# Optimization experiments

Measured on AMD Instinct MI355X. Metric: run time of the kernel, lower is better.

The kernel has to match this reference:

```python
import jax, jax.numpy as jnp
import numpy as np
from jax import lax

NK, NV, DK, DV, K, C = 16, 32, 128, 128, 4, 2048
KEY_DIM = NK * DK
VAL_DIM = NV * DV
CONV_DIM = 2 * KEY_DIM + VAL_DIM
EPS = 1e-6


def setup_inputs() -> dict:
    key = jax.random.key(0)
    ks = jax.random.split(key, 10)
    B, T = 2, 2048
    s = 0.02
    return {
        "x": jax.random.normal(ks[0], (B, T, C), jnp.float32),
        "input_pos": jnp.arange(T, dtype=jnp.int32),
        "W_qkv": jax.random.normal(ks[1], (CONV_DIM, C), jnp.float32) * s,
        "W_z": jax.random.normal(ks[2], (VAL_DIM, C), jnp.float32) * s,
        "W_b": jax.random.normal(ks[3], (NV, C), jnp.float32) * s,
        "W_a": jax.random.normal(ks[4], (NV, C), jnp.float32) * s,
        "conv_w": jax.random.normal(ks[5], (CONV_DIM, 1, K), jnp.float32) * 0.1,
        "dt_bias": jnp.ones((NV,), jnp.float32),
        "A_log": jnp.log(jax.random.uniform(ks[6], (NV,), jnp.float32, 1e-3, 16.0)),
        "norm_w": jnp.ones((DV,), jnp.float32),
        "W_out": jax.random.normal(ks[7], (C, VAL_DIM), jnp.float32) * s,
        "conv_state": jnp.zeros((B, CONV_DIM, K), jnp.float32),
        "recurrent_state": jnp.zeros((B, NV, DK, DV), jnp.float32),
    }


def reference(x, input_pos, W_qkv, W_z, W_b, W_a, conv_w, dt_bias, A_log,
              norm_w, W_out, conv_state, recurrent_state):
    B, T, _ = x.shape
    # reset cached state when starting a new sequence (input_pos[0] == 0)
    keep = 1.0 - (input_pos[0] == 0).astype(x.dtype)
    conv_state = conv_state * keep
    state0 = recurrent_state * keep

    qkv = jnp.einsum('btc,dc->btd', x, W_qkv)                      # [B,T,CONV_DIM]
    z = jnp.einsum('btc,dc->btd', x, W_z).reshape(B, T, NV, DV)
    beta = jax.nn.sigmoid(jnp.einsum('btc,hc->bth', x, W_b))       # [B,T,NV]
    a = jnp.einsum('btc,hc->bth', x, W_a)
    g = -jnp.exp(A_log) * jax.nn.softplus(a + dt_bias)             # [B,T,NV]

    # causal depthwise conv using cached conv_state as left context
    conv_in = jnp.concatenate([conv_state, qkv.transpose(0, 2, 1)], axis=-1)  # [B,D,K+T]
    conv_out = lax.conv_general_dilated(
        conv_in, conv_w, (1,), 'VALID',
        dimension_numbers=('NCH', 'OIH', 'NCH'),
        feature_group_count=CONV_DIM)
    qkv_c = jax.nn.silu(conv_out[:, :, -T:]).transpose(0, 2, 1)    # [B,T,CONV_DIM]

    q = qkv_c[..., :KEY_DIM].reshape(B, T, NK, DK)
    k = qkv_c[..., KEY_DIM:2 * KEY_DIM].reshape(B, T, NK, DK)
    v = qkv_c[..., 2 * KEY_DIM:].reshape(B, T, NV, DV)
    q = q / jnp.maximum(jnp.linalg.norm(q, axis=-1, keepdims=True), 1e-12)
    k = k / jnp.maximum(jnp.linalg.norm(k, axis=-1, keepdims=True), 1e-12)
    rep = NV // NK
    if rep > 1:
        q = jnp.repeat(q, rep, axis=2)
        k = jnp.repeat(k, rep, axis=2)

    # gated delta-rule recurrence over time
    def step(carry, xs):
        q_i, k_i, v_i, g_i, b_i = xs                               # [B,H,*]
        new = (jnp.exp(g_i)[..., None, None] * carry
               + b_i[..., None, None] * (k_i[..., :, None] * v_i[..., None, :]))
        out = jnp.einsum('bhk,bhkv->bhv', q_i, new)
        return new, out

    xs = (q.transpose(1, 0, 2, 3), k.transpose(1, 0, 2, 3),
          v.transpose(1, 0, 2, 3), g.transpose(1, 0, 2), beta.transpose(1, 0, 2))
    state, outs = lax.scan(step, state0, xs)
    o = outs.transpose(1, 0, 2, 3)                                 # [B,T,NV,DV]

    # gated RMSNorm (Mamba2-style): gate with silu(z), then RMS-normalize
    o = o * jax.nn.silu(z)
    var = jnp.mean(o * o, axis=-1, keepdims=True)
    o = o * lax.rsqrt(var + EPS) * norm_w
    return jnp.einsum('btd,cd->btc', o.reshape(B, T, VAL_DIM), W_out)
```

## Files before the change

### kernel.cpp

```cpp
#include <hip/hip_runtime.h>
#include <hip/hip_bf16.h>
#include <math.h>

#define NKH 16
#define NVH 32
#define DKD 128
#define DVD 128
#define CDIM 2048
#define KEY_DIM 2048
#define VAL_DIM 4096
#define CONV_DIM 8192
#define BB 2
#define TT 2048
#define MROWS 4096
#define CH 64
#define NCHUNK 32

typedef unsigned short u16;
typedef __bf16 bf16x8 __attribute__((ext_vector_type(8)));
typedef float f32x4 __attribute__((ext_vector_type(4)));

__device__ __forceinline__ u16 f2bf(float f) {
    union { float f; unsigned u; } a; a.f = f;
    unsigned u = a.u;
    u += 0x7fffu + ((u >> 16) & 1u);
    return (u16)(u >> 16);
}
__device__ __forceinline__ float bf2f(u16 h) {
    union { unsigned u; float f; } a; a.u = ((unsigned)h) << 16;
    return a.f;
}
union BF8 { bf16x8 v; uint2 u2[2]; uint4 u4; u16 s[8]; };
__device__ __forceinline__ bf16x8 lds_ld8(const u16* p) {
    BF8 t; t.u2[0] = *(const uint2*)p; t.u2[1] = *(const uint2*)(p + 4); return t.v;
}
__device__ __forceinline__ bf16x8 lds_ld16(const u16* p) {
    BF8 t; t.u4 = *(const uint4*)p; return t.v;
}
__device__ __forceinline__ void lds_st8(u16* p, uint4 v) {
    *(uint2*)p = make_uint2(v.x, v.y); *(uint2*)(p + 4) = make_uint2(v.z, v.w);
}

__device__ __forceinline__ void xcd_swizzle(int& tx, int& ty) {
    const int nx = gridDim.x, ny = gridDim.y;
    const int b  = blockIdx.x + nx * blockIdx.y;
    const int nb = nx * ny;
    if (nx >= 8 && (nx & 7) == 0 && (nb & 255) == 0) {
        const int rnd  = b >> 8;
        const int idx  = b & 255;
        const int xcd  = idx & 7;
        const int slot = idx >> 3;
        const int RX   = nx >> 3;
        const int rx   = xcd & (RX - 1);
        const int ry   = xcd >> __popc(RX - 1);
        tx = rx * 8 + (slot & 7);
        ty = rnd * (256 / nx) + ry * 4 + (slot >> 3);
    } else {
        tx = blockIdx.x; ty = blockIdx.y;
    }
}

__global__ __launch_bounds__(256) void fill_kernel(float* __restrict__ p, float v, int n) {
    int i = blockIdx.x * 256 + threadIdx.x;
    if (i < n) p[i] = v;
}

__global__ __launch_bounds__(256) void cast_kernel(const float* __restrict__ src,
                                                   u16* __restrict__ dst, int n4) {
    int i = blockIdx.x * 256 + threadIdx.x;
    if (i >= n4) return;
    float4 v = ((const float4*)src)[i];
    ushort4 r;
    r.x = f2bf(v.x); r.y = f2bf(v.y); r.z = f2bf(v.z); r.w = f2bf(v.w);
    ((ushort4*)dst)[i] = r;
}

template<int OUT_BF16>
__global__ __launch_bounds__(256) void gemm_nt(const u16* __restrict__ A,
                                               const u16* __restrict__ Bm,
                                               void* __restrict__ Cv,
                                               int M, int N, int K) {
    __shared__ __align__(16) u16 As[128 * 64];
    __shared__ __align__(16) u16 Bs[128 * 64];
    const int tid  = threadIdx.x;
    const int lane = tid & 63;
    const int wave = tid >> 6;
    int tx, ty;
    xcd_swizzle(tx, ty);
    const int m0 = ty * 128;
    const int n0 = tx * 128;
    const int wm = (wave & 1) * 64;
    const int wn = (wave >> 1) * 64;
    const int l15  = lane & 15;
    const int quad = lane >> 4;

    f32x4 acc[4][4];
#pragma unroll
    for (int i = 0; i < 4; ++i)
#pragma unroll
        for (int j = 0; j < 4; ++j) acc[i][j] = (f32x4)0.0f;

    const int crow = tid >> 3;
    const int ccol = (tid & 7) * 8;

    for (int k0 = 0; k0 < K; k0 += 64) {
#pragma unroll
        for (int p = 0; p < 4; ++p) {
            int row = p * 32 + crow;
            const u16* ga = A + (size_t)(m0 + row) * K + k0 + ccol;
            char* la = (char*)As + (size_t)(p * 256 + (wave << 6)) * 16;
            __builtin_amdgcn_global_load_lds((const __attribute__((address_space(1))) void*)ga,
                                             (__attribute__((address_space(3))) void*)la, 16, 0, 0);
            const u16* gb = Bm + (size_t)(n0 + row) * K + k0 + ccol;
            char* lb = (char*)Bs + (size_t)(p * 256 + (wave << 6)) * 16;
            __builtin_amdgcn_global_load_lds((const __attribute__((address_space(1))) void*)gb,
                                             (__attribute__((address_space(3))) void*)lb, 16, 0, 0);
        }
        __syncthreads();
#pragma unroll
        for (int kk = 0; kk < 64; kk += 32) {
            bf16x8 af[4], bfr[4];
#pragma unroll
            for (int i = 0; i < 4; ++i) {
                af[i]  = *(const bf16x8*)&As[(wm + i * 16 + l15) * 64 + kk + quad * 8];
                bfr[i] = *(const bf16x8*)&Bs[(wn + i * 16 + l15) * 64 + kk + quad * 8];
            }
#pragma unroll
            for (int i = 0; i < 4; ++i)
#pragma unroll
                for (int j = 0; j < 4; ++j)
                    acc[i][j] = __builtin_amdgcn_mfma_f32_16x16x32_bf16(af[i], bfr[j], acc[i][j], 0, 0, 0);
        }
        __syncthreads();
    }
#pragma unroll
    for (int i = 0; i < 4; ++i) {
#pragma unroll
        for (int j = 0; j < 4; ++j) {
#pragma unroll
            for (int r = 0; r < 4; ++r) {
                int grow = m0 + wm + i * 16 + quad * 4 + r;
                int gcol = n0 + wn + j * 16 + l15;
                if (OUT_BF16) {
                    ((u16*)Cv)[(size_t)grow * N + gcol] = f2bf(acc[i][j][r]);
                } else {
                    ((float*)Cv)[(size_t)grow * N + gcol] = acc[i][j][r];
                }
            }
        }
    }
}

template<int OUT_BF16>
__global__ __launch_bounds__(512, 2) void gemm_nt_256(const u16* __restrict__ A,
                                                      const u16* __restrict__ Bm,
                                                      void* __restrict__ Cv,
                                                      int M, int N, int K) {
    __shared__ __align__(16) u16 sA[2][256 * 64];
    __shared__ __align__(16) u16 sB[2][256 * 64];
    const int tid  = threadIdx.x;
    const int lane = tid & 63;
    const int wave = tid >> 6;
    const int wr   = wave >> 2;
    const int wc   = wave & 3;
    const int l15  = lane & 15;
    const int quad = lane >> 4;
    int tx, ty;
    xcd_swizzle(tx, ty);
    const int m0 = ty * 256;
    const int n0 = tx * 256;

    f32x4 acc[8][4];
#pragma unroll
    for (int i = 0; i < 8; ++i)
#pragma unroll
        for (int j = 0; j < 4; ++j) acc[i][j] = (f32x4)0.0f;

    auto stage = [&](int buf, int kk0) {
#pragma unroll
        for (int p = 0; p < 4; ++p) {
            const int gbase = p * 512 + wave * 64;
            const int g   = gbase + lane;
            const int row = g >> 3;
            const int sc  = (g & 7) ^ (row & 7);
            const u16* ga = A + (size_t)(m0 + row) * K + kk0 + sc * 8;
            __builtin_amdgcn_global_load_lds(
                (const __attribute__((address_space(1))) void*)ga,
                (__attribute__((address_space(3))) void*)((char*)&sA[buf][0] + (size_t)gbase * 16),
                16, 0, 0);
            const u16* gb = Bm + (size_t)(n0 + row) * K + kk0 + sc * 8;
            __builtin_amdgcn_global_load_lds(
                (const __attribute__((address_space(1))) void*)gb,
                (__attribute__((address_space(3))) void*)((char*)&sB[buf][0] + (size_t)gbase * 16),
                16, 0, 0);
        }
    };

    const int NT = K >> 6;
    stage(0, 0);

    for (int T = 0; T < NT; ++T) {
        const int P = T & 1;
        __builtin_amdgcn_sched_barrier(0);
        asm volatile("s_waitcnt vmcnt(0)" ::: "memory");
        __builtin_amdgcn_s_barrier();
        __builtin_amdgcn_sched_barrier(0);
        if (T + 1 < NT) stage(P ^ 1, (T + 1) << 6);

        bf16x8 bB[4][2];
#pragma unroll
        for (int j = 0; j < 4; ++j)
#pragma unroll
            for (int kk = 0; kk < 2; ++kk) {
                int row  = wc * 64 + j * 16 + l15;
                int slot = ((kk * 4 + quad) ^ (l15 & 7)) * 8;
                bB[j][kk] = lds_ld16(&sB[P][row * 64 + slot]);
            }
        bf16x8 aC[2][2], aN[2][2];
#pragma unroll
        for (int i = 0; i < 2; ++i)
#pragma unroll
            for (int kk = 0; kk < 2; ++kk) {
                int row  = wr * 128 + i * 16 + l15;
                int slot = ((kk * 4 + quad) ^ (l15 & 7)) * 8;
                aC[i][kk] = lds_ld16(&sA[P][row * 64 + slot]);
            }

#pragma unroll
        for (int q = 0; q < 4; ++q) {
            if (q < 3) {
#pragma unroll
                for (int i = 0; i < 2; ++i)
#pragma unroll
                    for (int kk = 0; kk < 2; ++kk) {
                        int row  = wr * 128 + ((q + 1) * 2 + i) * 16 + l15;
                        int slot = ((kk * 4 + quad) ^ (l15 & 7)) * 8;
                        aN[i][kk] = lds_ld16(&sA[P][row * 64 + slot]);
                    }
            }
            __builtin_amdgcn_s_setprio(1);
#pragma unroll
            for (int i = 0; i < 2; ++i)
#pragma unroll
                for (int j = 0; j < 4; ++j)
#pragma unroll
                    for (int kk = 0; kk < 2; ++kk)
                        acc[q * 2 + i][j] = __builtin_amdgcn_mfma_f32_16x16x32_bf16(
                            aC[i][kk], bB[j][kk], acc[q * 2 + i][j], 0, 0, 0);
            __builtin_amdgcn_s_setprio(0);
            __builtin_amdgcn_sched_barrier(0);
            if (q < 3) {
                __builtin_amdgcn_s_barrier();
#pragma unroll
                for (int i = 0; i < 2; ++i)
#pragma unroll
                    for (int kk = 0; kk < 2; ++kk) aC[i][kk] = aN[i][kk];
            }
        }
    }

#pragma unroll
    for (int i = 0; i < 8; ++i) {
#pragma unroll
        for (int j = 0; j < 4; ++j) {
#pragma unroll
            for (int r = 0; r < 4; ++r) {
                int grow = m0 + wr * 128 + i * 16 + quad * 4 + r;
                int gcol = n0 + wc * 64 + j * 16 + l15;
                if (OUT_BF16) {
                    ((u16*)Cv)[(size_t)grow * N + gcol] = f2bf(acc[i][j][r]);
                } else {
                    ((float*)Cv)[(size_t)grow * N + gcol] = acc[i][j][r];
                }
            }
        }
    }
}

__global__ __launch_bounds__(256) void bg_epilogue(const float* __restrict__ scores,
                                                   const float* __restrict__ dt_bias,
                                                   const float* __restrict__ A_log,
                                                   float* __restrict__ beta,
                                                   float* __restrict__ g) {
    int i = blockIdx.x * 256 + threadIdx.x;
    int row = i >> 6, col = i & 63;
    float s = scores[(size_t)row * 128 + col];
    if (col < 32) {
        beta[(size_t)row * 32 + col] = 1.f / (1.f + __expf(-s));
    } else {
        int h = col - 32;
        float aa = s + dt_bias[h];
        float sp = (aa > 20.f) ? aa : log1pf(__expf(aa));
        g[(size_t)row * 32 + h] = -__expf(A_log[h]) * sp;
    }
}

__global__ __launch_bounds__(256) void conv_silu_kernel(const u16* __restrict__ qkv,
                                                        const float* __restrict__ conv_w,
                                                        const float* __restrict__ conv_state,
                                                        const int* __restrict__ input_pos,
                                                        u16* __restrict__ qkvc) {
    const int d   = blockIdx.x * 256 + threadIdx.x;
    const int row = blockIdx.y;
    const int t   = row & (TT - 1);
    const int b   = row >> 11;
    const float keep = (input_pos[0] == 0) ? 0.f : 1.f;
    float4 w = *(const float4*)&conv_w[(size_t)d * 4];
    float acc = 0.f;
#pragma unroll
    for (int j = 0; j < 4; ++j) {
        int u = t + j - 3;
        float v;
        if (u >= 0) v = bf2f(qkv[(size_t)(b * TT + u) * CONV_DIM + d]);
        else        v = keep * conv_state[((size_t)b * CONV_DIM + d) * 4 + (u + 4)];
        acc += (&w.x)[j] * v;
    }
    float s = acc / (1.f + __expf(-acc));
    qkvc[(size_t)row * CONV_DIM + d] = f2bf(s);
}

__global__ __launch_bounds__(256) void qknorm_kernel(u16* __restrict__ qkvc) {
    const int gid  = blockIdx.x * 4 + (threadIdx.x >> 6);
    const int lane = threadIdx.x & 63;
    const int row  = gid >> 5;
    const int h    = gid & 31;
    u16* p = qkvc + (size_t)row * CONV_DIM + h * 128;
    ushort2 vb = *(ushort2*)&p[lane * 2];
    float v0 = bf2f(vb.x), v1 = bf2f(vb.y);
    float ss = v0 * v0 + v1 * v1;
#pragma unroll
    for (int off = 32; off; off >>= 1) ss += __shfl_xor(ss, off);
    float scale = 1.f / fmaxf(sqrtf(ss), 1e-12f);
    ushort2 r;
    r.x = f2bf(v0 * scale);
    r.y = f2bf(v1 * scale);
    *(ushort2*)&p[lane * 2] = r;
}

__global__ __launch_bounds__(64) void gates_kernel(const float* __restrict__ g,
                                                   const float* __restrict__ beta_,
                                                   float* __restrict__ gcum,
                                                   float* __restrict__ qsb,
                                                   float* __restrict__ wkb,
                                                   float* __restrict__ dLb) {
    const int bh = blockIdx.x, c = blockIdx.y;
    const int b = bh >> 5, h = bh & 31;
    const int t = threadIdx.x;
    const int row = b * TT + c * CH + t;
    float G = g[(size_t)row * 32 + h];
#pragma unroll
    for (int off = 1; off < 64; off <<= 1) {
        float x = __shfl_up(G, off);
        if (t >= off) G += x;
    }
    float GL = __shfl(G, 63);
    int oidx = bh * TT + c * CH + t;
    gcum[oidx] = G;
    qsb[oidx] = __expf(G);
    wkb[oidx] = __expf(GL - G) * beta_[(size_t)row * 32 + h];
    if (t == 0) dLb[bh * NCHUNK + c] = __expf(GL);
}

__global__ __launch_bounds__(256) void ktrans_kernel(const u16* __restrict__ qkvc,
                                                     u16* __restrict__ kT) {
    const int id = blockIdx.x;
    const int tt = id & 31, dkh = (id >> 5) & 1, hk = (id >> 6) & 15, b = id >> 10;
    const int t0 = tt * 64, dk0 = dkh * 64;
    __shared__ __align__(16) u16 tile[64 * 68];
#pragma unroll
    for (int it = 0; it < 2; ++it) {
        int idx = it * 256 + threadIdx.x;
        int tl = idx >> 3, c8 = (idx & 7) * 8;
        uint4 v = *(const uint4*)&qkvc[(size_t)(b * TT + t0 + tl) * CONV_DIM + KEY_DIM + hk * 128 + dk0 + c8];
        lds_st8(&tile[tl * 68 + c8], v);
    }
    __syncthreads();
#pragma unroll
    for (int it = 0; it < 2; ++it) {
        int idx = it * 256 + threadIdx.x;
        int dkl = idx >> 3, t8 = (idx & 7) * 8;
        unsigned w[4];
#pragma unroll
        for (int p = 0; p < 4; ++p) {
            unsigned lo = tile[(t8 + 2 * p) * 68 + dkl];
            unsigned hi = tile[(t8 + 2 * p + 1) * 68 + dkl];
            w[p] = lo | (hi << 16);
        }
        *(uint4*)&kT[((size_t)((b * 16 + hk) * 128 + dk0 + dkl)) * TT + t0 + t8] =
            make_uint4(w[0], w[1], w[2], w[3]);
    }
}

__global__ __launch_bounds__(256) void chunk_state_kernel(const u16* __restrict__ qkvc,
                                                          const u16* __restrict__ kT,
                                                          const float* __restrict__ qsb,
                                                          const float* __restrict__ wkb,
                                                          const float* __restrict__ dLb,
                                                          const float* __restrict__ rec_state,
                                                          const int* __restrict__ input_pos,
                                                          u16* __restrict__ o) {
    const int b = blockIdx.x, h = blockIdx.y, dvs = blockIdx.z;
    const int tid = threadIdx.x, lane = tid & 63, wave = tid >> 6;
    const int l15 = lane & 15, quad = lane >> 4;
    const int hq = h >> 1, bh = b * 32 + h;
    const float keep = (input_pos[0] == 0) ? 0.f : 1.f;

    __shared__ __align__(16) u16 sQ[64 * 132];
    __shared__ __align__(16) u16 sKT[128 * 68];
    __shared__ __align__(16) u16 sR[32 * 132];
    __shared__ float sQS[64];

    f32x4 st[2][2];
#pragma unroll
    for (int i = 0; i < 2; ++i)
#pragma unroll
        for (int j = 0; j < 2; ++j)
#pragma unroll
            for (int r = 0; r < 4; ++r) {
                int dv = dvs * 32 + i * 16 + quad * 4 + r;
                int dk = wave * 32 + j * 16 + l15;
                st[i][j][r] = keep * rec_state[((size_t)(bh * 128 + dk)) * 128 + dv];
            }

    for (int c = 0; c < NCHUNK; ++c) {
        const int t0 = c * CH;
#pragma unroll
        for (int i = 0; i < 2; ++i)
#pragma unroll
            for (int j = 0; j < 2; ++j)
#pragma unroll
                for (int r = 0; r < 4; ++r)
                    sR[(i * 16 + quad * 4 + r) * 132 + wave * 32 + j * 16 + l15] = f2bf(st[i][j][r]);
#pragma unroll
        for (int it = 0; it < 4; ++it) {
            int idx = it * 256 + tid;
            int t = idx >> 4, c8 = (idx & 15) * 8;
            uint4 v = *(const uint4*)&qkvc[(size_t)(b * TT + t0 + t) * CONV_DIM + hq * 128 + c8];
            lds_st8(&sQ[t * 132 + c8], v);
        }
        if (tid < 64) sQS[tid] = qsb[bh * TT + t0 + tid];
        __syncthreads();
        {
            f32x4 ao[2] = {(f32x4)0.0f, (f32x4)0.0f};
#pragma unroll
            for (int kk = 0; kk < 4; ++kk) {
                bf16x8 af = lds_ld8(&sQ[(wave * 16 + l15) * 132 + kk * 32 + quad * 8]);
                bf16x8 b0 = lds_ld8(&sR[(l15) * 132 + kk * 32 + quad * 8]);
                bf16x8 b1 = lds_ld8(&sR[(16 + l15) * 132 + kk * 32 + quad * 8]);
                ao[0] = __builtin_amdgcn_mfma_f32_16x16x32_bf16(af, b0, ao[0], 0, 0, 0);
                ao[1] = __builtin_amdgcn_mfma_f32_16x16x32_bf16(af, b1, ao[1], 0, 0, 0);
            }
#pragma unroll
            for (int j = 0; j < 2; ++j)
#pragma unroll
                for (int r = 0; r < 4; ++r) {
                    int t = wave * 16 + quad * 4 + r;
                    int dv = dvs * 32 + j * 16 + l15;
                    o[((size_t)(b * TT + t0 + t) * 32 + h) * 128 + dv] = f2bf(ao[j][r] * sQS[t]);
                }
        }
        __syncthreads();
#pragma unroll
        for (int it = 0; it < 4; ++it) {
            int idx = it * 256 + tid;
            int dk = idx >> 3, t8 = (idx & 7) * 8;
            uint4 v = *(const uint4*)&kT[((size_t)((b * 16 + hq) * 128 + dk)) * TT + t0 + t8];
            lds_st8(&sKT[dk * 68 + t8], v);
        }
        {
            int t = tid >> 2, dvo = (tid & 3) * 8;
            float w = wkb[bh * TT + t0 + t];
            BF8 v;
            v.u4 = *(const uint4*)&qkvc[(size_t)(b * TT + t0 + t) * CONV_DIM + 2 * KEY_DIM + h * 128 + dvs * 32 + dvo];
#pragma unroll
            for (int u = 0; u < 8; ++u)
                sR[(dvo + u) * 68 + t] = f2bf(bf2f(v.s[u]) * w);
        }
        __syncthreads();
        {
            float d = dLb[bh * NCHUNK + c];
#pragma unroll
            for (int i = 0; i < 2; ++i)
#pragma unroll
                for (int j = 0; j < 2; ++j)
#pragma unroll
                    for (int r = 0; r < 4; ++r) st[i][j][r] *= d;
#pragma unroll
            for (int kk = 0; kk < 2; ++kk) {
                bf16x8 af[2], bfv[2];
#pragma unroll
                for (int i = 0; i < 2; ++i)
                    af[i] = lds_ld8(&sR[(i * 16 + l15) * 68 + kk * 32 + quad * 8]);
#pragma unroll
                for (int j = 0; j < 2; ++j)
                    bfv[j] = lds_ld8(&sKT[(wave * 32 + j * 16 + l15) * 68 + kk * 32 + quad * 8]);
#pragma unroll
                for (int i = 0; i < 2; ++i)
#pragma unroll
                    for (int j = 0; j < 2; ++j)
                        st[i][j] = __builtin_amdgcn_mfma_f32_16x16x32_bf16(af[i], bfv[j], st[i][j], 0, 0, 0);
            }
        }
        __syncthreads();
    }
}

__global__ __launch_bounds__(256) void chunk_intra_kernel(const u16* __restrict__ qkvc,
                                                          const float* __restrict__ gcum,
                                                          const float* __restrict__ beta_,
                                                          u16* __restrict__ o) {
    const int b = blockIdx.x, h = blockIdx.y, c = blockIdx.z;
    const int tid = threadIdx.x, lane = tid & 63, wave = tid >> 6;
    const int l15 = lane & 15, quad = lane >> 4;
    const int hq = h >> 1, bh = b * 32 + h;
    const int t0 = c * CH;

    __shared__ __align__(16) u16 sQ[64 * 132];
    __shared__ __align__(16) u16 sK[64 * 132];
    __shared__ __align__(16) u16 sVT[128 * 68];
    __shared__ float sG[64];
    __shared__ float sB[64];

#pragma unroll
    for (int it = 0; it < 4; ++it) {
        int idx = it * 256 + tid;
        int t = idx >> 4, c8 = (idx & 15) * 8;
        size_t rbase = (size_t)(b * TT + t0 + t) * CONV_DIM;
        lds_st8(&sQ[t * 132 + c8], *(const uint4*)&qkvc[rbase + hq * 128 + c8]);
        lds_st8(&sK[t * 132 + c8], *(const uint4*)&qkvc[rbase + KEY_DIM + hq * 128 + c8]);
    }
    if (tid < 64) {
        sG[tid] = gcum[bh * TT + t0 + tid];
        sB[tid] = beta_[(size_t)(b * TT + t0 + tid) * 32 + h];
    }
    __syncthreads();
    const int wm = (wave & 1) * 32, wn = (wave >> 1) * 32;
    f32x4 acc[2][2];
#pragma unroll
    for (int i = 0; i < 2; ++i)
#pragma unroll
        for (int j = 0; j < 2; ++j) acc[i][j] = (f32x4)0.0f;
#pragma unroll
    for (int kk = 0; kk < 4; ++kk) {
        bf16x8 af[2], bfv[2];
#pragma unroll
        for (int i = 0; i < 2; ++i) {
            af[i]  = lds_ld8(&sQ[(wm + i * 16 + l15) * 132 + kk * 32 + quad * 8]);
            bfv[i] = lds_ld8(&sK[(wn + i * 16 + l15) * 132 + kk * 32 + quad * 8]);
        }
#pragma unroll
        for (int i = 0; i < 2; ++i)
#pragma unroll
            for (int j = 0; j < 2; ++j)
                acc[i][j] = __builtin_amdgcn_mfma_f32_16x16x32_bf16(af[i], bfv[j], acc[i][j], 0, 0, 0);
    }
    __syncthreads();
#pragma unroll
    for (int i = 0; i < 2; ++i)
#pragma unroll
        for (int j = 0; j < 2; ++j)
#pragma unroll
            for (int r = 0; r < 4; ++r) {
                int t = wm + i * 16 + quad * 4 + r;
                int s = wn + j * 16 + l15;
                float av = 0.f;
                if (s <= t) av = __expf(sG[t] - sG[s]) * sB[s] * acc[i][j][r];
                ((u16*)sQ)[t * 68 + s] = f2bf(av);
            }
#pragma unroll
    for (int it = 0; it < 4; ++it) {
        int idx = it * 256 + tid;
        int t = idx >> 4, c8 = (idx & 15) * 8;
        lds_st8(&sK[t * 132 + c8],
                *(const uint4*)&qkvc[(size_t)(b * TT + t0 + t) * CONV_DIM + 2 * KEY_DIM + h * 128 + c8]);
    }
    __syncthreads();
    {
        int dv = (wave & 1) * 64 + lane;
        int tb = (wave >> 1) * 32;
#pragma unroll
        for (int tc = 0; tc < 4; ++tc) {
            int t8 = tb + tc * 8;
            unsigned w[4];
#pragma unroll
            for (int p = 0; p < 4; ++p) {
                unsigned lo = sK[(t8 + 2 * p) * 132 + dv];
                unsigned hi = sK[(t8 + 2 * p + 1) * 132 + dv];
                w[p] = lo | (hi << 16);
            }
            lds_st8(&sVT[dv * 68 + t8], make_uint4(w[0], w[1], w[2], w[3]));
        }
    }
    __syncthreads();
    const int wm2 = (wave & 1) * 32, wn2 = (wave >> 1) * 64;
    f32x4 oacc[2][4];
#pragma unroll
    for (int i = 0; i < 2; ++i)
#pragma unroll
        for (int j = 0; j < 4; ++j) oacc[i][j] = (f32x4)0.0f;
#pragma unroll
    for (int kk = 0; kk < 2; ++kk) {
        bf16x8 af[2], bfv[4];
#pragma unroll
        for (int i = 0; i < 2; ++i)
            af[i] = lds_ld8(&((u16*)sQ)[(wm2 + i * 16 + l15) * 68 + kk * 32 + quad * 8]);
#pragma unroll
        for (int j = 0; j < 4; ++j)
            bfv[j] = lds_ld8(&sVT[(wn2 + j * 16 + l15) * 68 + kk * 32 + quad * 8]);
#pragma unroll
        for (int i = 0; i < 2; ++i)
#pragma unroll
            for (int j = 0; j < 4; ++j)
                oacc[i][j] = __builtin_amdgcn_mfma_f32_16x16x32_bf16(af[i], bfv[j], oacc[i][j], 0, 0, 0);
    }
#pragma unroll
    for (int i = 0; i < 2; ++i)
#pragma unroll
        for (int j = 0; j < 4; ++j)
#pragma unroll
            for (int r = 0; r < 4; ++r) {
                int t = wm2 + i * 16 + quad * 4 + r;
                int dv = wn2 + j * 16 + l15;
                size_t addr = ((size_t)(b * TT + t0 + t) * 32 + h) * 128 + dv;
                o[addr] = f2bf(oacc[i][j][r] + bf2f(o[addr]));
            }
}

__global__ __launch_bounds__(256) void gnorm_kernel(const u16* __restrict__ o,
                                                    const u16* __restrict__ zb,
                                                    const float* __restrict__ norm_w,
                                                    u16* __restrict__ ob) {
    const int gid  = blockIdx.x * 4 + (threadIdx.x >> 6);
    const int lane = threadIdx.x & 63;
    const int row  = gid >> 5;
    const int h    = gid & 31;
    const size_t base = ((size_t)row * NVH + h) * DVD;
    ushort2 oraw = *(const ushort2*)&o[base + lane * 2];
    float o0 = bf2f(oraw.x), o1 = bf2f(oraw.y);
    float z0 = bf2f(zb[base + lane * 2]);
    float z1 = bf2f(zb[base + lane * 2 + 1]);
    o0 *= z0 / (1.f + __expf(-z0));
    o1 *= z1 / (1.f + __expf(-z1));
    float ss = o0 * o0 + o1 * o1;
#pragma unroll
    for (int off = 32; off; off >>= 1) ss += __shfl_xor(ss, off);
    float scale = rsqrtf(ss * (1.f / 128.f) + 1e-6f);
    float w0 = norm_w[lane * 2], w1 = norm_w[lane * 2 + 1];
    ushort2 r;
    r.x = f2bf(o0 * scale * w0);
    r.y = f2bf(o1 * scale * w1);
    *(ushort2*)&ob[base + lane * 2] = r;
}

extern "C" void kernel_launch(void* const* d_in, const int* in_sizes, int n_in,
                              void* d_out, int out_size, void* d_ws, size_t ws_size,
                              hipStream_t stream) {
    const float* x         = (const float*)d_in[0];
    const int*   input_pos = (const int*)d_in[1];
    const float* W_qkv     = (const float*)d_in[2];
    const float* W_z       = (const float*)d_in[3];
    const float* W_b       = (const float*)d_in[4];
    const float* W_a       = (const float*)d_in[5];
    const float* conv_w    = (const float*)d_in[6];
    const float* dt_bias   = (const float*)d_in[7];
    const float* A_log     = (const float*)d_in[8];
    const float* norm_w    = (const float*)d_in[9];
    const float* W_out     = (const float*)d_in[10];
    const float* conv_state = (const float*)d_in[11];
    const float* rec_state  = (const float*)d_in[12];
    float* out = (float*)d_out;

    const size_t REQUIRED = 168820736;
    if (ws_size < REQUIRED) {
        float mib = (float)((double)ws_size / 1048576.0);
        fill_kernel<<<(out_size + 255) / 256, 256, 0, stream>>>(out, mib, out_size);
        return;
    }

    const size_t MI = 1048576;
    char* ws = (char*)d_ws;
    u16* xb    = (u16*)(ws);
    u16* wqkvb = (u16*)(ws + 16 * MI);
    u16* wzb   = (u16*)(ws + 48 * MI);
    u16* wbab  = (u16*)(ws + 16 * MI);
    float* bgs = (float*)(ws + 17 * MI);
    u16* qkvc  = (u16*)(ws);
    u16* ob    = (u16*)(ws);
    u16* woutb = (u16*)(ws + 32 * MI);
    u16* zb    = (u16*)(ws + 64 * MI);
    u16* qkvb  = (u16*)(ws + 96 * MI);
    u16* o     = (u16*)(ws + 96 * MI);
    u16* kT    = (u16*)(ws + 128 * MI);
    float* gcum = (float*)(ws + 144 * MI);
    float* qsb  = (float*)(ws + 144 * MI + 524288);
    float* wkb  = (float*)(ws + 145 * MI);
    float* dLb  = (float*)(ws + 145 * MI + 524288);
    float* beta = (float*)(ws + 160 * MI);
    float* g    = (float*)(ws + 160 * MI + 524288);

    cast_kernel<<<8192,  256, 0, stream>>>(x,     xb,    2097152);
    cast_kernel<<<16384, 256, 0, stream>>>(W_qkv, wqkvb, 4194304);
    cast_kernel<<<8192,  256, 0, stream>>>(W_z,   wzb,   2097152);

    gemm_nt_256<1><<<dim3(32, 16), 512, 0, stream>>>(xb, wqkvb, qkvb, MROWS, CONV_DIM, CDIM);
    gemm_nt_256<1><<<dim3(16, 16), 512, 0, stream>>>(xb, wzb,   zb,   MROWS, VAL_DIM,  CDIM);

    cast_kernel<<<256, 256, 0, stream>>>(W_b, wbab, 16384);
    cast_kernel<<<256, 256, 0, stream>>>(W_a, wbab + 65536, 16384);
    hipMemsetAsync(wbab + 131072, 0, 131072 * sizeof(u16), stream);
    gemm_nt<0><<<dim3(1, 32), 256, 0, stream>>>(xb, wbab, bgs, MROWS, 128, CDIM);
    bg_epilogue<<<1024, 256, 0, stream>>>(bgs, dt_bias, A_log, beta, g);

    conv_silu_kernel<<<dim3(32, 4096), 256, 0, stream>>>(qkvb, conv_w, conv_state, input_pos, qkvc);
    qknorm_kernel<<<32768, 256, 0, stream>>>(qkvc);

    gates_kernel<<<dim3(64, NCHUNK), 64, 0, stream>>>(g, beta, gcum, qsb, wkb, dLb);
    ktrans_kernel<<<2048, 256, 0, stream>>>(qkvc, kT);
    chunk_state_kernel<<<dim3(BB, NVH, 4), 256, 0, stream>>>(qkvc, kT, qsb, wkb, dLb,
                                                             rec_state, input_pos, o);
    chunk_intra_kernel<<<dim3(BB, NVH, NCHUNK), 256, 0, stream>>>(qkvc, gcum, beta, o);

    cast_kernel<<<8192, 256, 0, stream>>>(W_out, woutb, 2097152);
    gnorm_kernel<<<32768, 256, 0, stream>>>(o, zb, norm_w, ob);

    gemm_nt<0><<<dim3(16, 32), 256, 0, stream>>>(ob, woutb, out, MROWS, CDIM, VAL_DIM);
}
```

Before: 790.4 us.

## Pipeline 256-tile GEMM with split half-stage loads and swizzle 128-tile LDS

The 256x256 GEMM now loads A and B in half-tiles, interleaved between the MFMA quarter-steps, and prefetches up to two K-steps ahead using a partial vmcnt wait instead of draining all loads each iteration. Wave row ownership changes to interleaved 64-row strips, and the epilogue row mapping is updated to match. The 128-tile GEMM also gets an XOR swizzle on its LDS layout to reduce bank conflicts on fragment reads. The aim is to hide global-load latency and cut LDS conflicts, at the cost of more barriers and tighter, more fragile buffer-reuse ordering.

```diff
diff --git a/kernel.cpp b/kernel.cpp
--- a/kernel.cpp
+++ b/kernel.cpp
@@ -101,17 +101,17 @@
         for (int j = 0; j < 4; ++j) acc[i][j] = (f32x4)0.0f;
 
     const int crow = tid >> 3;
-    const int ccol = (tid & 7) * 8;
+    const int scol = ((tid & 7) ^ (crow & 7)) * 8;
 
     for (int k0 = 0; k0 < K; k0 += 64) {
 #pragma unroll
         for (int p = 0; p < 4; ++p) {
             int row = p * 32 + crow;
-            const u16* ga = A + (size_t)(m0 + row) * K + k0 + ccol;
+            const u16* ga = A + (size_t)(m0 + row) * K + k0 + scol;
             char* la = (char*)As + (size_t)(p * 256 + (wave << 6)) * 16;
             __builtin_amdgcn_global_load_lds((const __attribute__((address_space(1))) void*)ga,
                                              (__attribute__((address_space(3))) void*)la, 16, 0, 0);
-            const u16* gb = Bm + (size_t)(n0 + row) * K + k0 + ccol;
+            const u16* gb = Bm + (size_t)(n0 + row) * K + k0 + scol;
             char* lb = (char*)Bs + (size_t)(p * 256 + (wave << 6)) * 16;
             __builtin_amdgcn_global_load_lds((const __attribute__((address_space(1))) void*)gb,
                                              (__attribute__((address_space(3))) void*)lb, 16, 0, 0);
@@ -122,8 +122,9 @@
             bf16x8 af[4], bfr[4];
 #pragma unroll
             for (int i = 0; i < 4; ++i) {
-                af[i]  = *(const bf16x8*)&As[(wm + i * 16 + l15) * 64 + kk + quad * 8];
-                bfr[i] = *(const bf16x8*)&Bs[(wn + i * 16 + l15) * 64 + kk + quad * 8];
+                int sa = (((kk >> 3) + quad) ^ (l15 & 7)) * 8;
+                af[i]  = *(const bf16x8*)&As[(wm + i * 16 + l15) * 64 + sa];
+                bfr[i] = *(const bf16x8*)&Bs[(wn + i * 16 + l15) * 64 + sa];
             }
 #pragma unroll
             for (int i = 0; i < 4; ++i)
@@ -150,6 +151,21 @@
         }
     }
 }
+
+#define MFMA_Q(Q, AF) do {                                                      \
+    __builtin_amdgcn_s_setprio(1);                                              \
+    _Pragma("unroll")                                                           \
+    for (int i_ = 0; i_ < 2; ++i_)                                              \
+        _Pragma("unroll")                                                       \
+        for (int j_ = 0; j_ < 4; ++j_)                                          \
+            _Pragma("unroll")                                                   \
+            for (int kk_ = 0; kk_ < 2; ++kk_)                                   \
+                acc[(Q) * 2 + i_][j_] = __builtin_amdgcn_mfma_f32_16x16x32_bf16(\
+                    AF[i_][kk_], bB[j_][kk_], acc[(Q) * 2 + i_][j_], 0, 0, 0);  \
+    __builtin_amdgcn_s_setprio(0); } while (0)
+
+#define SBAR __builtin_amdgcn_s_barrier()
+#define SGB  __builtin_amdgcn_sched_barrier(0)
 
 template<int OUT_BF16>
 __global__ __launch_bounds__(512, 2) void gemm_nt_256(const u16* __restrict__ A,
@@ -176,19 +192,28 @@
 #pragma unroll
         for (int j = 0; j < 4; ++j) acc[i][j] = (f32x4)0.0f;
 
-    auto stage = [&](int buf, int kk0) {
-#pragma unroll
-        for (int p = 0; p < 4; ++p) {
-            const int gbase = p * 512 + wave * 64;
+    auto stageA = [&](int buf, int half, int k0) {
+#pragma unroll
+        for (int p = 0; p < 2; ++p) {
+            const int gbase = half * 1024 + p * 512 + wave * 64;
             const int g   = gbase + lane;
             const int row = g >> 3;
-            const int sc  = (g & 7) ^ (row & 7);
-            const u16* ga = A + (size_t)(m0 + row) * K + kk0 + sc * 8;
+            const int sc  = ((g & 7) ^ (row & 7)) * 8;
+            const u16* ga = A + (size_t)(m0 + row) * K + k0 + sc;
             __builtin_amdgcn_global_load_lds(
                 (const __attribute__((address_space(1))) void*)ga,
                 (__attribute__((address_space(3))) void*)((char*)&sA[buf][0] + (size_t)gbase * 16),
                 16, 0, 0);
-            const u16* gb = Bm + (size_t)(n0 + row) * K + kk0 + sc * 8;
+        }
+    };
+    auto stageB = [&](int buf, int half, int k0) {
+#pragma unroll
+        for (int p = 0; p < 2; ++p) {
+            const int gbase = half * 1024 + p * 512 + wave * 64;
+            const int g   = gbase + lane;
+            const int row = g >> 3;
+            const int sc  = ((g & 7) ^ (row & 7)) * 8;
+            const u16* gb = Bm + (size_t)(n0 + row) * K + k0 + sc;
             __builtin_amdgcn_global_load_lds(
                 (const __attribute__((address_space(1))) void*)gb,
                 (__attribute__((address_space(3))) void*)((char*)&sB[buf][0] + (size_t)gbase * 16),
@@ -197,17 +222,22 @@
     };
 
     const int NT = K >> 6;
-    stage(0, 0);
+    stageB(0, 0, 0); stageA(0, 0, 0); stageA(0, 1, 0); stageB(0, 1, 0);
+    if (NT > 1) { stageB(1, 0, 64); stageA(1, 0, 64); stageA(1, 1, 64); }
 
     for (int T = 0; T < NT; ++T) {
-        const int P = T & 1;
-        __builtin_amdgcn_sched_barrier(0);
-        asm volatile("s_waitcnt vmcnt(0)" ::: "memory");
-        __builtin_amdgcn_s_barrier();
-        __builtin_amdgcn_sched_barrier(0);
-        if (T + 1 < NT) stage(P ^ 1, (T + 1) << 6);
-
-        bf16x8 bB[4][2];
+        const int P  = T & 1;
+        const int k1 = (T + 1) << 6, k2 = (T + 2) << 6;
+        const bool s1 = (T + 1 < NT), s2 = (T + 2 < NT);
+
+        SGB;
+        if (s1) asm volatile("s_waitcnt vmcnt(6)" ::: "memory");
+        else    asm volatile("s_waitcnt vmcnt(0)" ::: "memory");
+        SGB;
+        SBAR;
+        SGB;
+
+        bf16x8 bB[4][2], aX[2][2], aY[2][2];
 #pragma unroll
         for (int j = 0; j < 4; ++j)
 #pragma unroll
@@ -216,61 +246,60 @@
                 int slot = ((kk * 4 + quad) ^ (l15 & 7)) * 8;
                 bB[j][kk] = lds_ld16(&sB[P][row * 64 + slot]);
             }
-        bf16x8 aC[2][2], aN[2][2];
 #pragma unroll
         for (int i = 0; i < 2; ++i)
 #pragma unroll
             for (int kk = 0; kk < 2; ++kk) {
-                int row  = wr * 128 + i * 16 + l15;
                 int slot = ((kk * 4 + quad) ^ (l15 & 7)) * 8;
-                aC[i][kk] = lds_ld16(&sA[P][row * 64 + slot]);
-            }
-
-#pragma unroll
-        for (int q = 0; q < 4; ++q) {
-            if (q < 3) {
-#pragma unroll
-                for (int i = 0; i < 2; ++i)
-#pragma unroll
-                    for (int kk = 0; kk < 2; ++kk) {
-                        int row  = wr * 128 + ((q + 1) * 2 + i) * 16 + l15;
-                        int slot = ((kk * 4 + quad) ^ (l15 & 7)) * 8;
-                        aN[i][kk] = lds_ld16(&sA[P][row * 64 + slot]);
+                aX[i][kk] = lds_ld16(&sA[P][(0 * 64 + wr * 32 + i * 16 + l15) * 64 + slot]);
+                aY[i][kk] = lds_ld16(&sA[P][(1 * 64 + wr * 32 + i * 16 + l15) * 64 + slot]);
+            }
+        if (s1) stageB(P ^ 1, 1, k1);
+        SGB; SBAR;
+        MFMA_Q(0, aX);
+        SGB; SBAR;
+#pragma unroll
+        for (int i = 0; i < 2; ++i)
+#pragma unroll
+            for (int kk = 0; kk < 2; ++kk) {
+                int slot = ((kk * 4 + quad) ^ (l15 & 7)) * 8;
+                aX[i][kk] = lds_ld16(&sA[P][(2 * 64 + wr * 32 + i * 16 + l15) * 64 + slot]);
+            }
+        if (s2) stageB(P, 0, k2);
+        SGB; SBAR;
+        MFMA_Q(1, aY);
+        SGB; SBAR;
+#pragma unroll
+        for (int i = 0; i < 2; ++i)
+#pragma unroll
+            for (int kk = 0; kk < 2; ++kk) {
+                int slot = ((kk * 4 + quad) ^ (l15 & 7)) * 8;
+                aY[i][kk] = lds_ld16(&sA[P][(3 * 64 + wr * 32 + i * 16 + l15) * 64 + slot]);
+            }
+        if (s2) stageA(P, 0, k2);
+        SGB; SBAR;
+        MFMA_Q(2, aX);
+        SGB; SBAR;
+        MFMA_Q(3, aY);
+        SGB; SBAR;
+        if (s2) stageA(P, 1, k2);
+    }
+
+#pragma unroll
+    for (int q = 0; q < 4; ++q) {
+#pragma unroll
+        for (int i = 0; i < 2; ++i) {
+#pragma unroll
+            for (int j = 0; j < 4; ++j) {
+#pragma unroll
+                for (int r = 0; r < 4; ++r) {
+                    int grow = m0 + q * 64 + wr * 32 + i * 16 + quad * 4 + r;
+                    int gcol = n0 + wc * 64 + j * 16 + l15;
+                    if (OUT_BF16) {
+                        ((u16*)Cv)[(size_t)grow * N + gcol] = f2bf(acc[q * 2 + i][j][r]);
+                    } else {
+                        ((float*)Cv)[(size_t)grow * N + gcol] = acc[q * 2 + i][j][r];
                     }
-            }
-            __builtin_amdgcn_s_setprio(1);
-#pragma unroll
-            for (int i = 0; i < 2; ++i)
-#pragma unroll
-                for (int j = 0; j < 4; ++j)
-#pragma unroll
-                    for (int kk = 0; kk < 2; ++kk)
-                        acc[q * 2 + i][j] = __builtin_amdgcn_mfma_f32_16x16x32_bf16(
-                            aC[i][kk], bB[j][kk], acc[q * 2 + i][j], 0, 0, 0);
-            __builtin_amdgcn_s_setprio(0);
-            __builtin_amdgcn_sched_barrier(0);
-            if (q < 3) {
-                __builtin_amdgcn_s_barrier();
-#pragma unroll
-                for (int i = 0; i < 2; ++i)
-#pragma unroll
-                    for (int kk = 0; kk < 2; ++kk) aC[i][kk] = aN[i][kk];
-            }
-        }
-    }
-
-#pragma unroll
-    for (int i = 0; i < 8; ++i) {
-#pragma unroll
-        for (int j = 0; j < 4; ++j) {
-#pragma unroll
-            for (int r = 0; r < 4; ++r) {
-                int grow = m0 + wr * 128 + i * 16 + quad * 4 + r;
-                int gcol = n0 + wc * 64 + j * 16 + l15;
-                if (OUT_BF16) {
-                    ((u16*)Cv)[(size_t)grow * N + gcol] = f2bf(acc[i][j][r]);
-                } else {
-                    ((float*)Cv)[(size_t)grow * N + gcol] = acc[i][j][r];
                 }
             }
         }
```

After: 762.3 us. -3.6%, faster.
